# Optimization experiments

Hardware: AMD Instinct MI355X
Metric: run time of the kernel (lower is better)

The kernel has to match this reference:

```python
import jax, jax.numpy as jnp
import numpy as np

N_NODES = 100000
N_EDGES = 1600000
IN_DIM = 128
OUT_DIM = 64
SLOPE = 0.2


def setup_inputs() -> dict:
    key = jax.random.key(0)
    k1, k2, k3, k4 = jax.random.split(key, 4)
    h = jax.random.normal(k1, (N_NODES, IN_DIM), dtype=jnp.float32)
    W = jax.random.normal(k2, (OUT_DIM, IN_DIM), dtype=jnp.float32) * (1.0 / np.sqrt(IN_DIM))
    src = jax.random.randint(k3, (N_EDGES,), 0, N_NODES, dtype=jnp.int64)
    dst = jax.random.randint(k4, (N_EDGES,), 0, N_NODES, dtype=jnp.int64)
    return {"h": h, "W": W, "src": src, "dst": dst}


def reference(h, W, src, dst):
    n = h.shape[0]
    z = h @ W.T                                   # [N, out_dim]
    z_src = z[src]                                # [E, out_dim]
    z_dst = z[dst]                                # [E, out_dim]
    e = jax.nn.leaky_relu(jnp.sum(z_src * z_dst, axis=1), negative_slope=SLOPE)  # [E]
    # segment softmax over incoming edges of each destination node
    m = jax.ops.segment_max(e, dst, num_segments=n)        # [N], -inf for isolated nodes
    ex = jnp.exp(e - m[dst])                                # [E]
    denom = jax.ops.segment_sum(ex, dst, num_segments=n)    # [N]
    alpha = ex / denom[dst]                                 # [E]
    agg = jax.ops.segment_sum(alpha[:, None] * z_src, dst, num_segments=n)  # [N, out_dim]
    return jax.nn.elu(agg)
```

## Files before the change

### kernel.cpp

```cpp
#include <hip/hip_runtime.h>
#include <math.h>

#define SLOPE 0.2f
#define LOG2E 1.4426950408889634f

__global__ __launch_bounds__(256, 8) void gemm_hist_kernel(const float* __restrict__ h,
                                                           const float* __restrict__ W,
                                                           float* __restrict__ z,
                                                           const int* __restrict__ dst,
                                                           int* __restrict__ cnt,
                                                           int* __restrict__ rank,
                                                           int n, int ne) {
    int ei = blockIdx.x * 256 + threadIdx.x;
    int base = ei * 2;
    if (base + 1 < ne) {
        int2 d = *(const int2*)(dst + base);
        int2 r;
        r.x = atomicAdd(&cnt[d.x], 1);
        r.y = atomicAdd(&cnt[d.y], 1);
        *(int2*)(rank + base) = r;
    } else if (base < ne) {
        rank[base] = atomicAdd(&cnt[dst[base]], 1);
    }

    __shared__ float ws[128][36];
    int t = threadIdx.x;
    int nblk = blockIdx.x >> 1;
    int ch0  = (blockIdx.x & 1) << 5;
    const float4* __restrict__ W4 = reinterpret_cast<const float4*>(W);
#pragma unroll
    for (int j = 0; j < 4; j++) {
        int idx = t + j * 256;
        int o  = idx >> 5;
        int kq = idx & 31;
        float4 w = W4[(size_t)(ch0 + o) * 32 + kq];
        int k = kq << 2;
        int col = o ^ ((kq & 7) << 2);
        ws[k + 0][col] = w.x; ws[k + 1][col] = w.y;
        ws[k + 2][col] = w.z; ws[k + 3][col] = w.w;
    }
    __syncthreads();

    int ng = t >> 3, og = t & 7;
    int n0 = nblk * 64 + ng * 2;
    if (n0 >= n) return;
    const float* __restrict__ hp = h + (size_t)n0 * 128;

    float acc[2][4] = {};
#pragma unroll 4
    for (int k = 0; k < 128; k += 4) {
        int m = (k >> 2) & 7;
        int colb = (og ^ m) << 2;
        float4 hv[2], wv[4];
#pragma unroll
        for (int i = 0; i < 2; i++) hv[i] = *(const float4*)(hp + i * 128 + k);
#pragma unroll
        for (int kk = 0; kk < 4; kk++) wv[kk] = *(const float4*)&ws[k + kk][colb];
#pragma unroll
        for (int i = 0; i < 2; i++) {
            acc[i][0] += hv[i].x * wv[0].x + hv[i].y * wv[1].x + hv[i].z * wv[2].x + hv[i].w * wv[3].x;
            acc[i][1] += hv[i].x * wv[0].y + hv[i].y * wv[1].y + hv[i].z * wv[2].y + hv[i].w * wv[3].y;
            acc[i][2] += hv[i].x * wv[0].z + hv[i].y * wv[1].z + hv[i].z * wv[2].z + hv[i].w * wv[3].z;
            acc[i][3] += hv[i].x * wv[0].w + hv[i].y * wv[1].w + hv[i].z * wv[2].w + hv[i].w * wv[3].w;
        }
    }
#pragma unroll
    for (int i = 0; i < 2; i++) {
        *(float4*)&z[(size_t)(n0 + i) * 64 + ch0 + og * 4] =
            make_float4(acc[i][0], acc[i][1], acc[i][2], acc[i][3]);
    }
}

__global__ __launch_bounds__(256) void scan1(const int* __restrict__ cnt,
                                             int* __restrict__ starts,
                                             int* __restrict__ bsums, int n) {
    __shared__ int ls[256];
    int tbase = blockIdx.x * 4096 + threadIdx.x * 16;
    int v[16];
    int s = 0;
#pragma unroll
    for (int k = 0; k < 16; k++) {
        int idx = tbase + k;
        int c = idx < n ? cnt[idx] : 0;
        v[k] = c; s += c;
    }
    ls[threadIdx.x] = s;
    __syncthreads();
    for (int off = 1; off < 256; off <<= 1) {
        int t = threadIdx.x >= off ? ls[threadIdx.x - off] : 0;
        __syncthreads();
        ls[threadIdx.x] += t;
        __syncthreads();
    }
    int run = ls[threadIdx.x] - s;
    if (threadIdx.x == 255) bsums[blockIdx.x] = ls[255];
#pragma unroll
    for (int k = 0; k < 16; k++) {
        int idx = tbase + k;
        if (idx < n) starts[idx] = run;
        run += v[k];
    }
}

__global__ void scan2(int* __restrict__ bsums, int nb, int* __restrict__ starts,
                      int n, int ne) {
    if (threadIdx.x == 0) {
        int run = 0;
        for (int b = 0; b < nb; b++) { int t = bsums[b]; bsums[b] = run; run += t; }
        starts[n] = ne;
    }
}

__global__ __launch_bounds__(256) void scan3(int* __restrict__ starts,
                                             const int* __restrict__ bsums, int n) {
    int i = blockIdx.x * 256 + threadIdx.x;
    if (i < n) starts[i] += bsums[i >> 12];
}

__global__ __launch_bounds__(256) void scatter4_kernel(const int* __restrict__ src,
                                                       const int* __restrict__ dst,
                                                       const int* __restrict__ starts,
                                                       const int* __restrict__ rank,
                                                       int* __restrict__ csr_src, int ne) {
    int i = blockIdx.x * 256 + threadIdx.x;
    int base = i * 4;
    if (base + 3 < ne) {
        int4 s = *(const int4*)(src + base);
        int4 d = *(const int4*)(dst + base);
        int4 r = *(const int4*)(rank + base);
        csr_src[starts[d.x] + r.x] = s.x;
        csr_src[starts[d.y] + r.y] = s.y;
        csr_src[starts[d.z] + r.z] = s.z;
        csr_src[starts[d.w] + r.w] = s.w;
    } else {
        for (int r = base; r < ne; r++)
            csr_src[starts[dst[r]] + rank[r]] = src[r];
    }
}

__global__ __launch_bounds__(256) void fused_node(const float4* __restrict__ z4,
                                                  const int* __restrict__ starts,
                                                  const int* __restrict__ csr_src,
                                                  float4* __restrict__ out4, int n) {
    int node = blockIdx.x * 4 + (threadIdx.x >> 6);
    if (node >= n) return;
    int lane = threadIdx.x & 63;
    int g = lane >> 4;
    int q = lane & 15;
    int rs = starts[node], re = starts[node + 1];
    float4 zd = z4[(size_t)node * 16 + q];

    float m2 = -1e30f, denom = 0.f;
    float4 acc = make_float4(0.f, 0.f, 0.f, 0.f);

    for (int c = rs; c < re; c += 64) {
        int j = c + lane;
        int sv = j < re ? csr_src[j] : 0;
        int cn = min(64, re - c);
        int idx = g;
        bool val = idx < cn;
        int s = __shfl(sv, val ? idx : 0);
        float4 v = z4[(size_t)s * 16 + q];
        for (int k = 0; k < cn; k += 4) {
            int idx_n = k + 4 + g;
            bool val_n = idx_n < cn;
            int s_n = __shfl(sv, val_n ? idx_n : 0);
            float4 vn = z4[(size_t)s_n * 16 + q];
            float p = v.x * zd.x + v.y * zd.y + v.z * zd.z + v.w * zd.w;
#pragma unroll
            for (int msk = 1; msk < 16; msk <<= 1) p += __shfl_xor(p, msk);
            float e = p > 0.f ? p : SLOPE * p;
            float e2 = e * LOG2E;
            e2 = val ? e2 : -2e30f;
            if (__any(e2 > m2)) {
                float mnew = fmaxf(m2, e2);
                float sc = exp2f(m2 - mnew);
                float ex = exp2f(e2 - mnew);
                denom = fmaf(denom, sc, ex);
                acc.x = fmaf(acc.x, sc, ex * v.x);
                acc.y = fmaf(acc.y, sc, ex * v.y);
                acc.z = fmaf(acc.z, sc, ex * v.z);
                acc.w = fmaf(acc.w, sc, ex * v.w);
                m2 = mnew;
            } else {
                float ex = exp2f(e2 - m2);
                denom += ex;
                acc.x = fmaf(ex, v.x, acc.x);
                acc.y = fmaf(ex, v.y, acc.y);
                acc.z = fmaf(ex, v.z, acc.z);
                acc.w = fmaf(ex, v.w, acc.w);
            }
            v = vn; val = val_n;
        }
    }
#pragma unroll
    for (int msk = 16; msk < 64; msk <<= 1) {
        float mo  = __shfl_xor(m2, msk);
        float dno = __shfl_xor(denom, msk);
        float ax = __shfl_xor(acc.x, msk);
        float ay = __shfl_xor(acc.y, msk);
        float az = __shfl_xor(acc.z, msk);
        float aw = __shfl_xor(acc.w, msk);
        float mnew = fmaxf(m2, mo);
        float ss = exp2f(m2 - mnew), so = exp2f(mo - mnew);
        denom = fmaf(denom, ss, dno * so);
        acc.x = fmaf(acc.x, ss, ax * so);
        acc.y = fmaf(acc.y, ss, ay * so);
        acc.z = fmaf(acc.z, ss, az * so);
        acc.w = fmaf(acc.w, ss, aw * so);
        m2 = mnew;
    }
    if (lane < 16) {
        float inv = denom > 0.f ? 1.f / denom : 0.f;
        float4 r; float x;
        x = acc.x * inv; r.x = x > 0.f ? x : __expf(x) - 1.f;
        x = acc.y * inv; r.y = x > 0.f ? x : __expf(x) - 1.f;
        x = acc.z * inv; r.z = x > 0.f ? x : __expf(x) - 1.f;
        x = acc.w * inv; r.w = x > 0.f ? x : __expf(x) - 1.f;
        out4[(size_t)node * 16 + q] = r;
    }
}

extern "C" void kernel_launch(void* const* d_in, const int* in_sizes, int n_in,
                              void* d_out, int out_size, void* d_ws, size_t ws_size,
                              hipStream_t stream) {
    const float* h   = (const float*)d_in[0];
    const float* W   = (const float*)d_in[1];
    const int*   src = (const int*)d_in[2];
    const int*   dst = (const int*)d_in[3];
    int n  = in_sizes[0] / 128;
    int ne = in_sizes[2];

    float* z       = (float*)d_ws;
    int*   starts  = (int*)(z + (size_t)n * 64);
    int*   cnt     = starts + (n + 1);
    int*   rank    = cnt + n;
    int*   csr_src = rank + ne;
    int*   bsums   = csr_src + ne;

    int nb_gemm = ((n + 63) / 64) * 2;
    int nt4 = (ne + 3) / 4;
    int nb_scan = (n + 4095) / 4096;

    hipMemsetAsync(cnt, 0, (size_t)n * sizeof(int), stream);
    gemm_hist_kernel<<<nb_gemm, 256, 0, stream>>>(h, W, z, dst, cnt, rank, n, ne);
    scan1<<<nb_scan, 256, 0, stream>>>(cnt, starts, bsums, n);
    scan2<<<1, 64, 0, stream>>>(bsums, nb_scan, starts, n, ne);
    scan3<<<(n + 255) / 256, 256, 0, stream>>>(starts, bsums, n);
    scatter4_kernel<<<(nt4 + 255) / 256, 256, 0, stream>>>(src, dst, starts, rank,
                                                           csr_src, ne);
    fused_node<<<(n + 3) / 4, 256, 0, stream>>>((const float4*)z, starts, csr_src,
                                                (float4*)d_out, n);
}
```

Measured before the change: 205.7 us.

## Privatize histogram into 8 copies and scatter via atomic cursors without rank array

The destination-degree histogram is split across 8 per-block-group count arrays to reduce atomic contention. The per-edge rank array is dropped: scan3 turns each copy into a running cursor, and the scatter kernel claims slots with atomics. This removes the rank write and read traffic. In exchange it adds a second pass of atomics in the scatter, an 8x larger memset, and a scan that reads all 8 copies. Edge order within a node's CSR segment becomes nondeterministic, which changes float summation order.

```diff
diff --git a/kernel.cpp b/kernel.cpp
--- a/kernel.cpp
+++ b/kernel.cpp
@@ -8,19 +8,17 @@
                                                            const float* __restrict__ W,
                                                            float* __restrict__ z,
                                                            const int* __restrict__ dst,
-                                                           int* __restrict__ cnt,
-                                                           int* __restrict__ rank,
+                                                           int* __restrict__ cnt8,
                                                            int n, int ne) {
+    int* __restrict__ cnt = cnt8 + (size_t)(blockIdx.x & 7) * n;
     int ei = blockIdx.x * 256 + threadIdx.x;
     int base = ei * 2;
     if (base + 1 < ne) {
         int2 d = *(const int2*)(dst + base);
-        int2 r;
-        r.x = atomicAdd(&cnt[d.x], 1);
-        r.y = atomicAdd(&cnt[d.y], 1);
-        *(int2*)(rank + base) = r;
+        atomicAdd(&cnt[d.x], 1);
+        atomicAdd(&cnt[d.y], 1);
     } else if (base < ne) {
-        rank[base] = atomicAdd(&cnt[dst[base]], 1);
+        atomicAdd(&cnt[dst[base]], 1);
     }
 
     __shared__ float ws[128][36];
@@ -71,19 +69,35 @@
     }
 }
 
-__global__ __launch_bounds__(256) void scan1(const int* __restrict__ cnt,
+__global__ __launch_bounds__(256) void scan1(const int* __restrict__ cnt8,
                                              int* __restrict__ starts,
                                              int* __restrict__ bsums, int n) {
     __shared__ int ls[256];
     int tbase = blockIdx.x * 4096 + threadIdx.x * 16;
-    int v[16];
+    int tot[16];
+#pragma unroll
+    for (int k = 0; k < 16; k++) tot[k] = 0;
+    if (tbase + 15 < n) {
+#pragma unroll
+        for (int c = 0; c < 8; c++) {
+            const int* cp = cnt8 + (size_t)c * n + tbase;
+#pragma unroll
+            for (int q = 0; q < 4; q++) {
+                int4 v = *(const int4*)(cp + q * 4);
+                tot[q * 4 + 0] += v.x; tot[q * 4 + 1] += v.y;
+                tot[q * 4 + 2] += v.z; tot[q * 4 + 3] += v.w;
+            }
+        }
+    } else {
+        for (int k = 0; k < 16; k++) {
+            int idx = tbase + k;
+            if (idx < n)
+                for (int c = 0; c < 8; c++) tot[k] += cnt8[(size_t)c * n + idx];
+        }
+    }
     int s = 0;
 #pragma unroll
-    for (int k = 0; k < 16; k++) {
-        int idx = tbase + k;
-        int c = idx < n ? cnt[idx] : 0;
-        v[k] = c; s += c;
-    }
+    for (int k = 0; k < 16; k++) s += tot[k];
     ls[threadIdx.x] = s;
     __syncthreads();
     for (int off = 1; off < 256; off <<= 1) {
@@ -98,7 +112,7 @@
     for (int k = 0; k < 16; k++) {
         int idx = tbase + k;
         if (idx < n) starts[idx] = run;
-        run += v[k];
+        run += tot[k];
     }
 }
 
@@ -112,29 +126,37 @@
 }
 
 __global__ __launch_bounds__(256) void scan3(int* __restrict__ starts,
-                                             const int* __restrict__ bsums, int n) {
+                                             const int* __restrict__ bsums,
+                                             int* __restrict__ cnt8, int n) {
     int i = blockIdx.x * 256 + threadIdx.x;
-    if (i < n) starts[i] += bsums[i >> 12];
-}
-
-__global__ __launch_bounds__(256) void scatter4_kernel(const int* __restrict__ src,
+    if (i >= n) return;
+    int base = starts[i] + bsums[i >> 12];
+    starts[i] = base;
+#pragma unroll
+    for (int c = 0; c < 8; c++) {
+        size_t off = (size_t)c * n + i;
+        int t = cnt8[off];
+        cnt8[off] = base;
+        base += t;
+    }
+}
+
+__global__ __launch_bounds__(256) void scatter2_kernel(const int* __restrict__ src,
                                                        const int* __restrict__ dst,
-                                                       const int* __restrict__ starts,
-                                                       const int* __restrict__ rank,
-                                                       int* __restrict__ csr_src, int ne) {
-    int i = blockIdx.x * 256 + threadIdx.x;
-    int base = i * 4;
-    if (base + 3 < ne) {
-        int4 s = *(const int4*)(src + base);
-        int4 d = *(const int4*)(dst + base);
-        int4 r = *(const int4*)(rank + base);
-        csr_src[starts[d.x] + r.x] = s.x;
-        csr_src[starts[d.y] + r.y] = s.y;
-        csr_src[starts[d.z] + r.z] = s.z;
-        csr_src[starts[d.w] + r.w] = s.w;
-    } else {
-        for (int r = base; r < ne; r++)
-            csr_src[starts[dst[r]] + rank[r]] = src[r];
+                                                       int* __restrict__ cnt8,
+                                                       int* __restrict__ csr_src,
+                                                       int n, int ne) {
+    int* __restrict__ cur = cnt8 + (size_t)(blockIdx.x & 7) * n;
+    int ei = blockIdx.x * 256 + threadIdx.x;
+    int base = ei * 2;
+    if (base + 1 < ne) {
+        int2 s = *(const int2*)(src + base);
+        int2 d = *(const int2*)(dst + base);
+        int p0 = atomicAdd(&cur[d.x], 1); csr_src[p0] = s.x;
+        int p1 = atomicAdd(&cur[d.y], 1); csr_src[p1] = s.y;
+    } else if (base < ne) {
+        int p = atomicAdd(&cur[dst[base]], 1);
+        csr_src[p] = src[base];
     }
 }
 
@@ -232,23 +254,21 @@
     int ne = in_sizes[2];
 
     float* z       = (float*)d_ws;
-    int*   starts  = (int*)(z + (size_t)n * 64);
-    int*   cnt     = starts + (n + 1);
-    int*   rank    = cnt + n;
-    int*   csr_src = rank + ne;
-    int*   bsums   = csr_src + ne;
+    int*   cnt8    = (int*)(z + (size_t)n * 64);
+    int*   csr_src = cnt8 + (size_t)8 * n;
+    int*   starts  = csr_src + ne;
+    int*   bsums   = starts + ((n + 5) & ~3);
 
     int nb_gemm = ((n + 63) / 64) * 2;
-    int nt4 = (ne + 3) / 4;
+    int nb_edge = (ne / 2 + 255) / 256;
     int nb_scan = (n + 4095) / 4096;
 
-    hipMemsetAsync(cnt, 0, (size_t)n * sizeof(int), stream);
-    gemm_hist_kernel<<<nb_gemm, 256, 0, stream>>>(h, W, z, dst, cnt, rank, n, ne);
-    scan1<<<nb_scan, 256, 0, stream>>>(cnt, starts, bsums, n);
+    hipMemsetAsync(cnt8, 0, (size_t)8 * n * sizeof(int), stream);
+    gemm_hist_kernel<<<nb_gemm, 256, 0, stream>>>(h, W, z, dst, cnt8, n, ne);
+    scan1<<<nb_scan, 256, 0, stream>>>(cnt8, starts, bsums, n);
     scan2<<<1, 64, 0, stream>>>(bsums, nb_scan, starts, n, ne);
-    scan3<<<(n + 255) / 256, 256, 0, stream>>>(starts, bsums, n);
-    scatter4_kernel<<<(nt4 + 255) / 256, 256, 0, stream>>>(src, dst, starts, rank,
-                                                           csr_src, ne);
+    scan3<<<(n + 255) / 256, 256, 0, stream>>>(starts, bsums, cnt8, n);
+    scatter2_kernel<<<nb_edge, 256, 0, stream>>>(src, dst, cnt8, csr_src, n, ne);
     fused_node<<<(n + 3) / 4, 256, 0, stream>>>((const float4*)z, starts, csr_src,
                                                 (float4*)d_out, n);
 }
```

Result: slower. 305.9 us (+48.7%).
